# Optimization experiments

Hardware: AMD Instinct MI355X
Metric: run time of the kernel (lower is better)

Reference implementation:

```python
import jax, jax.numpy as jnp
import numpy as np

PC_RANGE = (-51.2, -51.2, -3.0, 51.2, 51.2, 1.0)
OUT = 3   # roi_align_size
SR = 2    # fixed sampling ratio (approximates mmcv adaptive sampling_ratio=0)


def roi_align_rotated(fm, rois_b, cx, cy, w, h, angle):
    """mmcv-style RoIAlignRotated, aligned=True, spatial_scale=1, clockwise=True.
    fm: [B,C,H,W]; rois_b int [N]; cx,cy,w,h,angle float [N]. Returns [N,C,OUT,OUT]."""
    B, C, H, W = fm.shape
    fm_hwc = jnp.transpose(fm, (0, 2, 3, 1))  # [B,H,W,C] for channel-last gather
    cx = cx - 0.5  # aligned=True pixel-center offset
    cy = cy - 0.5
    theta = -angle  # clockwise=True
    cos_t, sin_t = jnp.cos(theta), jnp.sin(theta)
    bin_h = h / OUT
    bin_w = w / OUT
    ph = jnp.arange(OUT, dtype=fm.dtype)
    sg = (jnp.arange(SR, dtype=fm.dtype) + 0.5) / SR
    # local (un-rotated) sample coords, [N, OUT, SR]
    yy = -h[:, None, None] / 2 + (ph[None, :, None] + sg[None, None, :]) * bin_h[:, None, None]
    xx = -w[:, None, None] / 2 + (ph[None, :, None] + sg[None, None, :]) * bin_w[:, None, None]
    # broadcast to [N, OUT(ph), OUT(pw), SR(iy), SR(ix)]
    yy = yy[:, :, None, :, None]
    xx = xx[:, None, :, None, :]
    c = cos_t[:, None, None, None, None]
    s = sin_t[:, None, None, None, None]
    y = yy * c - xx * s + cy[:, None, None, None, None]
    x = yy * s + xx * c + cx[:, None, None, None, None]
    N = cx.shape[0]
    P = OUT * OUT * SR * SR
    y = y.reshape(N, P)
    x = x.reshape(N, P)
    valid = (y > -1.0) & (y < H) & (x > -1.0) & (x < W)
    y = jnp.clip(y, 0.0, H - 1)
    x = jnp.clip(x, 0.0, W - 1)
    y0 = jnp.minimum(jnp.floor(y).astype(jnp.int32), H - 1)
    x0 = jnp.minimum(jnp.floor(x).astype(jnp.int32), W - 1)
    y1 = jnp.minimum(y0 + 1, H - 1)
    x1 = jnp.minimum(x0 + 1, W - 1)
    ly = y - y0
    lx = x - x0
    hy, hx = 1.0 - ly, 1.0 - lx
    bi = rois_b[:, None].astype(jnp.int32)
    v00 = fm_hwc[bi, y0, x0]  # [N,P,C]
    v01 = fm_hwc[bi, y0, x1]
    v10 = fm_hwc[bi, y1, x0]
    v11 = fm_hwc[bi, y1, x1]
    val = (hy * hx)[..., None] * v00 + (hy * lx)[..., None] * v01 \
        + (ly * hx)[..., None] * v10 + (ly * lx)[..., None] * v11
    val = val * valid[..., None].astype(fm.dtype)
    val = val.reshape(N, OUT, OUT, SR * SR, C).mean(axis=3)  # average over samples
    return jnp.transpose(val, (0, 3, 1, 2))  # [N,C,OUT,OUT]


def fc2(x, w1, w2):
    # two Conv1d(k=1, bias=False) + ReLU == two bias-free linears + ReLU
    return jax.nn.relu(jax.nn.relu(x @ w1.T) @ w2.T)


def setup_inputs() -> dict:
    key = jax.random.key(0)
    ks = jax.random.split(key, 20)
    B, C, H, W, N = 4, 256, 256, 256, 2048
    F = OUT * OUT * C  # 2304
    D = 256            # n_fc_neurons
    fm = jax.random.normal(ks[0], (B, C, H, W), jnp.float32)
    u = jax.random.uniform(ks[1], (N, 7), jnp.float32)
    boxes = jnp.stack([
        u[:, 0] * 90.0 - 45.0,        # x in [-45,45] m
        u[:, 1] * 90.0 - 45.0,        # y
        u[:, 2] * 2.0 - 2.0,          # z
        u[:, 3] * 4.5 + 1.5,          # h
        u[:, 4] * 4.5 + 1.5,          # w (roi height in pixels)
        u[:, 5] * 4.5 + 1.5,          # l (roi width in pixels)
        u[:, 6] * 2.0 * np.pi - np.pi  # yaw
    ], axis=1)
    bidx = jax.random.randint(ks[2], (N,), 0, B, dtype=jnp.int32)
    def mkw(k, o, i):
        return jax.random.normal(k, (o, i), jnp.float32) * np.float32(1.0 / np.sqrt(i))
    return {
        'feature_map': fm, 'boxes': boxes, 'batch_idx': bidx,
        'w_sh1': mkw(ks[3], D, F), 'w_sh2': mkw(ks[4], D, D),
        'w_cls1': mkw(ks[5], D, D), 'w_cls2': mkw(ks[6], D, D),
        'w_cls3': mkw(ks[7], 1, D), 'b_cls3': jnp.zeros((1,), jnp.float32),
        'w_iou1': mkw(ks[8], D, D), 'w_iou2': mkw(ks[9], D, D),
        'w_iou3': mkw(ks[10], 1, D), 'b_iou3': jnp.zeros((1,), jnp.float32),
        'w_reg1': mkw(ks[11], D, D), 'w_reg2': mkw(ks[12], D, D),
        'w_reg3': mkw(ks[13], 7, D) * np.float32(0.001), 'b_reg3': jnp.zeros((7,), jnp.float32),
    }


def reference(feature_map, boxes, batch_idx,
              w_sh1, w_sh2,
              w_cls1, w_cls2, w_cls3, b_cls3,
              w_iou1, w_iou2, w_iou3, b_iou3,
              w_reg1, w_reg2, w_reg3, b_reg3):
    H, W = feature_map.shape[2], feature_map.shape[3]
    gw = (PC_RANGE[3] - PC_RANGE[0]) / W
    gh = (PC_RANGE[4] - PC_RANGE[1]) / H
    cx = (boxes[:, 0] - PC_RANGE[0]) / gw
    cy = (boxes[:, 1] - PC_RANGE[1]) / gh
    rw = boxes[:, 5] / gw  # enlarge_ratio = 1
    rh = boxes[:, 4] / gh
    ang = boxes[:, 6]
    pooled = roi_align_rotated(feature_map, batch_idx, cx, cy, rw, rh, ang)  # [N,C,3,3]
    N, C = pooled.shape[0], pooled.shape[1]
    # flatten(2).permute(0,2,1).flatten(1): bin-major, channel-minor
    x = jnp.transpose(pooled.reshape(N, C, OUT * OUT), (0, 2, 1)).reshape(N, OUT * OUT * C)
    sh = fc2(x, w_sh1, w_sh2)
    rcnn_cls = fc2(sh, w_cls1, w_cls2) @ w_cls3.T + b_cls3
    rcnn_iou = fc2(sh, w_iou1, w_iou2) @ w_iou3.T + b_iou3
    rcnn_reg = fc2(sh, w_reg1, w_reg2) @ w_reg3.T + b_reg3
    return rcnn_cls, rcnn_iou, rcnn_reg
```

## Files before the change

### kernel.cpp

```cpp
#include <hip/hip_runtime.h>
#include <hip/hip_fp16.h>

typedef float f4v __attribute__((ext_vector_type(4)));
typedef _Float16 h4 __attribute__((ext_vector_type(4)));
typedef _Float16 h8 __attribute__((ext_vector_type(8)));

#define NROI 2048
#define NCH  256
#define MAPH 256
#define MAPW 256
#define HWSZ (MAPH*MAPW)
#define FDIM 2304
#define MN   (2048*256)

#define O_SH1 0
#define O_SH2 589824
#define O_C1  655360
#define O_C2  720896
#define O_I1  786432
#define O_I2  851968
#define O_R1  917504
#define O_R2  983040

__global__ __launch_bounds__(256) void convert_w_kernel(
    const float* __restrict__ s1, const float* __restrict__ s2,
    const float* __restrict__ c1, const float* __restrict__ c2,
    const float* __restrict__ i1, const float* __restrict__ i2,
    const float* __restrict__ r1, const float* __restrict__ r2,
    __half* __restrict__ wbuf)
{
    const int b = blockIdx.x, t = threadIdx.x;
    const float* src;
    int base;
    if (b < 1152) { src = s1 + (size_t)b*512; base = b*512; }
    else {
        int j  = (b - 1152) >> 7;
        int lb = (b - 1152) & 127;
        switch (j) {
            case 0: src = s2; break; case 1: src = c1; break;
            case 2: src = c2; break; case 3: src = i1; break;
            case 4: src = i2; break; case 5: src = r1; break;
            default: src = r2; break;
        }
        src += (size_t)lb*512;
        base = 589824 + (b - 1152)*512;
    }
    float2 v = *(const float2*)(src + t*2);
    *(__half2*)(wbuf + base + t*2) = __floats2half2_rn(v.x, v.y);
}

#define TP 136

__global__ __launch_bounds__(256) void transpose_kernel(
    const float* __restrict__ fm, __half* __restrict__ hwc)
{
    __shared__ _Float16 tile[128 * TP];
    const int tid = threadIdx.x;
    const int x0 = blockIdx.x * 128, c0 = blockIdx.y * 128;
    const int bz = blockIdx.z;
    const int b = bz >> 8, y = bz & 255;

    const int xh = tid & 31;
    const int cb = tid >> 5;
    const float* src = fm + (((size_t)b*NCH + c0 + cb)*MAPH + y)*MAPW + x0 + xh*4;
    const int swz = (xh & 15) << 2;
    const int xbase = xh * 4;

    #pragma unroll
    for (int p = 0; p < 16; p++) {
        f4v v = *(const f4v*)(src + (size_t)p*8*HWSZ);
        const int c = (cb + p*8) ^ swz;
        tile[(xbase+0)*TP + c] = (_Float16)v[0];
        tile[(xbase+1)*TP + c] = (_Float16)v[1];
        tile[(xbase+2)*TP + c] = (_Float16)v[2];
        tile[(xbase+3)*TP + c] = (_Float16)v[3];
    }
    __syncthreads();

    const int cq = tid & 31;
    const int xb = tid >> 5;
    __half* dst = hwc + (((size_t)b*MAPH + y)*MAPW + x0)*NCH + c0 + cq*4;
    #pragma unroll
    for (int it = 0; it < 16; it++) {
        int x = xb + it*8;
        h4 v = *(const h4*)&tile[x*TP + ((cq*4) ^ (((x>>2)&15) << 2))];
        *(h4*)(dst + (size_t)x*NCH) = v;
    }
}

__global__ __launch_bounds__(256) void roi_hwc_kernel(
    const __half* __restrict__ hwc, const float* __restrict__ boxes,
    const int* __restrict__ bidx, __half* __restrict__ xout)
{
    const int tid  = threadIdx.x;
    const int r    = tid >> 7;
    const int lt   = tid & 127;
    const int wq   = lt >> 6;
    const int lane = lt & 63;
    const int n    = blockIdx.x * 2 + r;

    __shared__ float sw[2][4][36];
    __shared__ int   soff[2][4][36];
    __shared__ int   sb[2];

    if (lt < 36) {
        float b0 = boxes[n*7+0], b1 = boxes[n*7+1];
        float b4 = boxes[n*7+4], b5 = boxes[n*7+5], b6 = boxes[n*7+6];
        float cx = (b0 + 51.2f) / 0.4f - 0.5f;
        float cy = (b1 + 51.2f) / 0.4f - 0.5f;
        float w  = b5 / 0.4f;
        float h  = b4 / 0.4f;
        float th = -b6;
        float ct = cosf(th), st = sinf(th);
        float binh = h / 3.0f, binw = w / 3.0f;
        int s  = lt;
        int ph = s / 12, pw = (s % 12) / 4, sy = (s % 4) / 2, sx = s & 1;
        float sgy = ((float)sy + 0.5f) * 0.5f;
        float sgx = ((float)sx + 0.5f) * 0.5f;
        float yy  = -h*0.5f + ((float)ph + sgy) * binh;
        float xxl = -w*0.5f + ((float)pw + sgx) * binw;
        float y = yy*ct - xxl*st + cy;
        float x = yy*st + xxl*ct + cx;
        bool valid = (y > -1.0f) && (y < 256.0f) && (x > -1.0f) && (x < 256.0f);
        y = fminf(fmaxf(y, 0.0f), 255.0f);
        x = fminf(fmaxf(x, 0.0f), 255.0f);
        int y0 = (int)floorf(y); if (y0 > 255) y0 = 255;
        int x0 = (int)floorf(x); if (x0 > 255) x0 = 255;
        int y1 = min(y0+1, 255), x1 = min(x0+1, 255);
        float ly = y - (float)y0, lx = x - (float)x0;
        float hy = 1.0f - ly, hx = 1.0f - lx;
        float v = valid ? 0.25f : 0.0f;
        sw[r][0][s] = hy*hx*v; sw[r][1][s] = hy*lx*v;
        sw[r][2][s] = ly*hx*v; sw[r][3][s] = ly*lx*v;
        soff[r][0][s] = (y0*MAPW + x0)*NCH;
        soff[r][1][s] = (y0*MAPW + x1)*NCH;
        soff[r][2][s] = (y1*MAPW + x0)*NCH;
        soff[r][3][s] = (y1*MAPW + x1)*NCH;
    }
    if (lt == 0) sb[r] = bidx[n];
    __syncthreads();

    const __half* base = hwc + (size_t)sb[r]*(HWSZ*NCH) + lane*4;
    __half* xo = xout + (size_t)n*FDIM + lane*4;

    for (int pp = wq; pp < 9; pp += 2) {
        float a0 = 0.f, a1 = 0.f, a2 = 0.f, a3 = 0.f;
        #pragma unroll
        for (int q = 0; q < 4; q++) {
            int s = pp*4 + q;
            #pragma unroll
            for (int cc = 0; cc < 4; cc++) {
                h4 v = *(const h4*)(base + soff[r][cc][s]);
                float wgt = sw[r][cc][s];
                a0 += wgt * (float)v[0];
                a1 += wgt * (float)v[1];
                a2 += wgt * (float)v[2];
                a3 += wgt * (float)v[3];
            }
        }
        h4 o; o[0]=(_Float16)a0; o[1]=(_Float16)a1; o[2]=(_Float16)a2; o[3]=(_Float16)a3;
        *(h4*)(xo + pp*NCH) = o;
    }
}

struct PtrsH {
    const __half* A[3];
    const __half* W[3];
    void* C[3];
};

__device__ inline h8 ldsH8(const _Float16* p) {
    h4 lo = *(const h4*)p;
    h4 hi = *(const h4*)(p + 4);
    return __builtin_shufflevector(lo, hi, 0,1,2,3,4,5,6,7);
}

template<bool RELU, bool SPLITK, bool OUTH>
__global__ __launch_bounds__(256) void gemm_h_kernel(PtrsH p, int M, int N, int K, int kChunk)
{
    __shared__ _Float16 As[64*40];
    __shared__ _Float16 Ws[64*40];
    const int z = blockIdx.z;
    const _Float16* A; const _Float16* W; void* C;
    int k0, k1;
    if (SPLITK) {
        A = (const _Float16*)p.A[0]; W = (const _Float16*)p.W[0];
        k0 = z * kChunk; k1 = k0 + kChunk;
        C = (char*)p.C[0] + (size_t)z * M * N * 4;
    } else {
        A = (const _Float16*)p.A[z]; W = (const _Float16*)p.W[z]; C = p.C[z];
        k0 = 0; k1 = K;
    }
    const int tid = threadIdx.x;
    const int m0 = blockIdx.x * 64, n0 = blockIdx.y * 64;
    const int srow = tid >> 2, skc = (tid & 3) * 8;
    const _Float16* Ald = A + (size_t)(m0 + srow) * K + k0 + skc;
    const _Float16* Wld = W + (size_t)(n0 + srow) * K + k0 + skc;
    const int wv = tid >> 6, lane = tid & 63;
    const int quad = lane >> 4, mr = lane & 15;

    f4v acc[4] = {};
    h8 aR = *(const h8*)Ald;
    h8 wR = *(const h8*)Wld;

    for (int kt = k0; kt < k1; kt += 32) {
        __syncthreads();
        *(h4*)&As[srow*40 + skc]     = __builtin_shufflevector(aR, aR, 0,1,2,3);
        *(h4*)&As[srow*40 + skc + 4] = __builtin_shufflevector(aR, aR, 4,5,6,7);
        *(h4*)&Ws[srow*40 + skc]     = __builtin_shufflevector(wR, wR, 0,1,2,3);
        *(h4*)&Ws[srow*40 + skc + 4] = __builtin_shufflevector(wR, wR, 4,5,6,7);
        __syncthreads();
        if (kt + 32 < k1) {
            Ald += 32; Wld += 32;
            aR = *(const h8*)Ald;
            wR = *(const h8*)Wld;
        }
        h8 af = ldsH8(&As[(wv*16 + mr)*40 + quad*8]);
        #pragma unroll
        for (int j = 0; j < 4; j++) {
            h8 bf = ldsH8(&Ws[(j*16 + mr)*40 + quad*8]);
            acc[j] = __builtin_amdgcn_mfma_f32_16x16x32_f16(af, bf, acc[j], 0, 0, 0);
        }
    }

    const int orow = m0 + wv*16 + quad*4;
    #pragma unroll
    for (int j = 0; j < 4; j++) {
        int col = n0 + j*16 + mr;
        #pragma unroll
        for (int rr = 0; rr < 4; rr++) {
            float v = acc[j][rr];
            if (RELU) v = fmaxf(v, 0.0f);
            if (OUTH) ((__half*)C)[(size_t)(orow + rr) * N + col] = __float2half(v);
            else      ((float*)C)[(size_t)(orow + rr) * N + col] = v;
        }
    }
}

__global__ __launch_bounds__(256) void reduce_relu_h_kernel(
    const float* __restrict__ pin, __half* __restrict__ hout)
{
    int i = blockIdx.x * 256 + threadIdx.x;
    const f4v* p4 = (const f4v*)pin;
    f4v a = p4[i];
    a += p4[i + MN/4];
    a += p4[i + 2*(MN/4)];
    a += p4[i + 3*(MN/4)];
    h4 o;
    #pragma unroll
    for (int j = 0; j < 4; j++) o[j] = (_Float16)fmaxf(a[j], 0.0f);
    *(h4*)(hout + (size_t)i*4) = o;
}

__global__ __launch_bounds__(256) void heads_kernel(
    const float* __restrict__ c2, const float* __restrict__ i2, const float* __restrict__ r2,
    const float* __restrict__ wc3, const float* __restrict__ bc3,
    const float* __restrict__ wi3, const float* __restrict__ bi3,
    const float* __restrict__ wr3, const float* __restrict__ br3,
    float* __restrict__ out)
{
    const int lane = threadIdx.x & 63;
    const int wv   = threadIdx.x >> 6;
    const int n    = blockIdx.x * 4 + wv;
    const float* cr = c2 + (size_t)n*256;
    const float* ir = i2 + (size_t)n*256;
    const float* rr = r2 + (size_t)n*256;
    float vc = 0.0f, vi = 0.0f, vr[7] = {};
    #pragma unroll
    for (int j = 0; j < 4; j++) {
        int k = lane + j*64;
        float cv = cr[k], iv = ir[k], rv = rr[k];
        vc += cv * wc3[k];
        vi += iv * wi3[k];
        #pragma unroll
        for (int t = 0; t < 7; t++) vr[t] += rv * wr3[t*256 + k];
    }
    #pragma unroll
    for (int off = 32; off > 0; off >>= 1) {
        vc += __shfl_down(vc, off, 64);
        vi += __shfl_down(vi, off, 64);
        #pragma unroll
        for (int t = 0; t < 7; t++) vr[t] += __shfl_down(vr[t], off, 64);
    }
    if (lane == 0) {
        out[n]        = vc + bc3[0];
        out[2048 + n] = vi + bi3[0];
        #pragma unroll
        for (int t = 0; t < 7; t++) out[4096 + n*7 + t] = vr[t] + br3[t];
    }
}

extern "C" void kernel_launch(void* const* d_in, const int* in_sizes, int n_in,
                              void* d_out, int out_size, void* d_ws, size_t ws_size,
                              hipStream_t stream)
{
    const float* fm    = (const float*)d_in[0];
    const float* boxes = (const float*)d_in[1];
    const int*   bidx  = (const int*)d_in[2];
    const float* w_sh1 = (const float*)d_in[3];
    const float* w_sh2 = (const float*)d_in[4];
    const float* w_c1  = (const float*)d_in[5];
    const float* w_c2  = (const float*)d_in[6];
    const float* w_c3  = (const float*)d_in[7];
    const float* b_c3  = (const float*)d_in[8];
    const float* w_i1  = (const float*)d_in[9];
    const float* w_i2  = (const float*)d_in[10];
    const float* w_i3  = (const float*)d_in[11];
    const float* b_i3  = (const float*)d_in[12];
    const float* w_r1  = (const float*)d_in[13];
    const float* w_r2  = (const float*)d_in[14];
    const float* w_r3  = (const float*)d_in[15];
    const float* b_r3  = (const float*)d_in[16];
    float* out = (float*)d_out;

    char* base = (char*)d_ws;
    __half* hwc  = (__half*)base;
    __half* xh   = (__half*)(base + (size_t)4*NCH*HWSZ*2);
    __half* h1h  = (__half*)((char*)xh + (size_t)NROI*FDIM*2);
    __half* shh  = (__half*)((char*)h1h + (size_t)MN*2);
    __half* b1c  = (__half*)((char*)shh + (size_t)MN*2);
    __half* b1i  = b1c + MN;
    __half* b1r  = b1i + MN;
    float*  b2c  = (float*)((char*)b1c + (size_t)3*MN*2);
    float*  b2i  = b2c + MN;
    float*  b2r  = b2i + MN;
    float*  part = (float*)((char*)b2c + (size_t)3*MN*4);
    __half* wbuf = (__half*)((char*)part + (size_t)4*MN*4);

    convert_w_kernel<<<2048, 256, 0, stream>>>(w_sh1, w_sh2, w_c1, w_c2,
                                               w_i1, w_i2, w_r1, w_r2, wbuf);
    transpose_kernel<<<dim3(2, 2, 4*MAPH), 256, 0, stream>>>(fm, hwc);
    roi_hwc_kernel<<<NROI/2, 256, 0, stream>>>(hwc, boxes, bidx, xh);

    PtrsH g1;
    g1.A[0]=g1.A[1]=g1.A[2]=xh;
    g1.W[0]=g1.W[1]=g1.W[2]=wbuf + O_SH1;
    g1.C[0]=g1.C[1]=g1.C[2]=part;
    gemm_h_kernel<false,true,false><<<dim3(32,4,4), 256, 0, stream>>>(g1, 2048, 256, 2304, 576);

    reduce_relu_h_kernel<<<MN/4/256, 256, 0, stream>>>(part, h1h);

    PtrsH g2;
    g2.A[0]=g2.A[1]=g2.A[2]=h1h;
    g2.W[0]=g2.W[1]=g2.W[2]=wbuf + O_SH2;
    g2.C[0]=g2.C[1]=g2.C[2]=shh;
    gemm_h_kernel<true,false,true><<<dim3(32,4,1), 256, 0, stream>>>(g2, 2048, 256, 256, 0);

    PtrsH g3;
    g3.A[0]=g3.A[1]=g3.A[2]=shh;
    g3.W[0]=wbuf + O_C1; g3.W[1]=wbuf + O_I1; g3.W[2]=wbuf + O_R1;
    g3.C[0]=b1c; g3.C[1]=b1i; g3.C[2]=b1r;
    gemm_h_kernel<true,false,true><<<dim3(32,4,3), 256, 0, stream>>>(g3, 2048, 256, 256, 0);

    PtrsH g4;
    g4.A[0]=b1c; g4.A[1]=b1i; g4.A[2]=b1r;
    g4.W[0]=wbuf + O_C2; g4.W[1]=wbuf + O_I2; g4.W[2]=wbuf + O_R2;
    g4.C[0]=b2c; g4.C[1]=b2i; g4.C[2]=b2r;
    gemm_h_kernel<true,false,false><<<dim3(32,4,3), 256, 0, stream>>>(g4, 2048, 256, 256, 0);

    heads_kernel<<<NROI/4, 256, 0, stream>>>(b2c, b2i, b2r,
                                             w_c3, b_c3, w_i3, b_i3, w_r3, b_r3, out);
}
```

Before: 472.1 us.

## Fuse final head projections into last GEMM epilogue with atomic accumulation

Removes the separate heads kernel and the fp32 intermediate buffers. The last hidden-layer GEMM now applies ReLU and immediately projects onto the final head weights in its epilogue. Partial sums are reduced across lanes and accumulated into the output with atomicAdd. Biases are written ahead of time by extra blocks in the weight-conversion kernel. This saves one launch and the write and read of the intermediate activations, at the cost of atomics, nondeterministic summation order and more register pressure in the reg-head epilogue.

```diff
diff --git a/kernel.cpp b/kernel.cpp
--- a/kernel.cpp
+++ b/kernel.cpp
@@ -27,9 +27,24 @@
     const float* __restrict__ c1, const float* __restrict__ c2,
     const float* __restrict__ i1, const float* __restrict__ i2,
     const float* __restrict__ r1, const float* __restrict__ r2,
-    __half* __restrict__ wbuf)
+    __half* __restrict__ wbuf,
+    const float* __restrict__ bc3, const float* __restrict__ bi3,
+    const float* __restrict__ br3, float* __restrict__ out)
 {
     const int b = blockIdx.x, t = threadIdx.x;
+    if (b >= 2048) {
+        int idx = (b - 2048) * 1024 + t * 4;
+        #pragma unroll
+        for (int k = 0; k < 4; k++) {
+            int i = idx + k;
+            float v;
+            if (i < 2048)      v = bc3[0];
+            else if (i < 4096) v = bi3[0];
+            else               v = br3[(i - 4096) % 7];
+            out[i] = v;
+        }
+        return;
+    }
     const float* src;
     int base;
     if (b < 1152) { src = s1 + (size_t)b*512; base = b*512; }
@@ -237,6 +252,103 @@
     }
 }
 
+__global__ __launch_bounds__(256) void gemm_heads_kernel(
+    const __half* __restrict__ Ac, const __half* __restrict__ Ai, const __half* __restrict__ Ar,
+    const __half* __restrict__ wbuf,
+    const float* __restrict__ wc3, const float* __restrict__ wi3, const float* __restrict__ wr3,
+    float* __restrict__ out)
+{
+    __shared__ _Float16 As[64*40];
+    __shared__ _Float16 Ws[64*40];
+    const int z = blockIdx.z;
+    const _Float16* A = (const _Float16*)(z == 0 ? Ac : (z == 1 ? Ai : Ar));
+    const _Float16* W = (const _Float16*)wbuf + (z == 0 ? O_C2 : (z == 1 ? O_I2 : O_R2));
+    const int K = 256;
+    const int tid = threadIdx.x;
+    const int m0 = blockIdx.x * 64, n0 = blockIdx.y * 64;
+    const int srow = tid >> 2, skc = (tid & 3) * 8;
+    const _Float16* Ald = A + (size_t)(m0 + srow) * K + skc;
+    const _Float16* Wld = W + (size_t)(n0 + srow) * K + skc;
+    const int wv = tid >> 6, lane = tid & 63;
+    const int quad = lane >> 4, mr = lane & 15;
+
+    f4v acc[4] = {};
+    h8 aR = *(const h8*)Ald;
+    h8 wR = *(const h8*)Wld;
+
+    for (int kt = 0; kt < K; kt += 32) {
+        __syncthreads();
+        *(h4*)&As[srow*40 + skc]     = __builtin_shufflevector(aR, aR, 0,1,2,3);
+        *(h4*)&As[srow*40 + skc + 4] = __builtin_shufflevector(aR, aR, 4,5,6,7);
+        *(h4*)&Ws[srow*40 + skc]     = __builtin_shufflevector(wR, wR, 0,1,2,3);
+        *(h4*)&Ws[srow*40 + skc + 4] = __builtin_shufflevector(wR, wR, 4,5,6,7);
+        __syncthreads();
+        if (kt + 32 < K) {
+            Ald += 32; Wld += 32;
+            aR = *(const h8*)Ald;
+            wR = *(const h8*)Wld;
+        }
+        h8 af = ldsH8(&As[(wv*16 + mr)*40 + quad*8]);
+        #pragma unroll
+        for (int j = 0; j < 4; j++) {
+            h8 bf = ldsH8(&Ws[(j*16 + mr)*40 + quad*8]);
+            acc[j] = __builtin_amdgcn_mfma_f32_16x16x32_f16(af, bf, acc[j], 0, 0, 0);
+        }
+    }
+
+    const int orow = m0 + wv*16 + quad*4;
+    if (z < 2) {
+        const float* w3 = (z == 0) ? wc3 : wi3;
+        float pc[4] = {0.f, 0.f, 0.f, 0.f};
+        #pragma unroll
+        for (int j = 0; j < 4; j++) {
+            float w3v = w3[n0 + j*16 + mr];
+            #pragma unroll
+            for (int rr = 0; rr < 4; rr++)
+                pc[rr] += fmaxf(acc[j][rr], 0.0f) * w3v;
+        }
+        #pragma unroll
+        for (int off = 1; off < 16; off <<= 1) {
+            #pragma unroll
+            for (int rr = 0; rr < 4; rr++)
+                pc[rr] += __shfl_xor(pc[rr], off, 64);
+        }
+        if (mr == 0) {
+            #pragma unroll
+            for (int rr = 0; rr < 4; rr++)
+                atomicAdd(out + z*2048 + orow + rr, pc[rr]);
+        }
+    } else {
+        float pr[4][7] = {};
+        #pragma unroll
+        for (int j = 0; j < 4; j++) {
+            int col = n0 + j*16 + mr;
+            #pragma unroll
+            for (int rr = 0; rr < 4; rr++) {
+                float v = fmaxf(acc[j][rr], 0.0f);
+                #pragma unroll
+                for (int t = 0; t < 7; t++)
+                    pr[rr][t] += v * wr3[t*256 + col];
+            }
+        }
+        #pragma unroll
+        for (int off = 1; off < 16; off <<= 1) {
+            #pragma unroll
+            for (int rr = 0; rr < 4; rr++)
+                #pragma unroll
+                for (int t = 0; t < 7; t++)
+                    pr[rr][t] += __shfl_xor(pr[rr][t], off, 64);
+        }
+        if (mr == 0) {
+            #pragma unroll
+            for (int rr = 0; rr < 4; rr++)
+                #pragma unroll
+                for (int t = 0; t < 7; t++)
+                    atomicAdd(out + 4096 + (size_t)(orow + rr)*7 + t, pr[rr][t]);
+        }
+    }
+}
+
 __global__ __launch_bounds__(256) void reduce_relu_h_kernel(
     const float* __restrict__ pin, __half* __restrict__ hout)
 {
@@ -250,44 +362,6 @@
     #pragma unroll
     for (int j = 0; j < 4; j++) o[j] = (_Float16)fmaxf(a[j], 0.0f);
     *(h4*)(hout + (size_t)i*4) = o;
-}
-
-__global__ __launch_bounds__(256) void heads_kernel(
-    const float* __restrict__ c2, const float* __restrict__ i2, const float* __restrict__ r2,
-    const float* __restrict__ wc3, const float* __restrict__ bc3,
-    const float* __restrict__ wi3, const float* __restrict__ bi3,
-    const float* __restrict__ wr3, const float* __restrict__ br3,
-    float* __restrict__ out)
-{
-    const int lane = threadIdx.x & 63;
-    const int wv   = threadIdx.x >> 6;
-    const int n    = blockIdx.x * 4 + wv;
-    const float* cr = c2 + (size_t)n*256;
-    const float* ir = i2 + (size_t)n*256;
-    const float* rr = r2 + (size_t)n*256;
-    float vc = 0.0f, vi = 0.0f, vr[7] = {};
-    #pragma unroll
-    for (int j = 0; j < 4; j++) {
-        int k = lane + j*64;
-        float cv = cr[k], iv = ir[k], rv = rr[k];
-        vc += cv * wc3[k];
-        vi += iv * wi3[k];
-        #pragma unroll
-        for (int t = 0; t < 7; t++) vr[t] += rv * wr3[t*256 + k];
-    }
-    #pragma unroll
-    for (int off = 32; off > 0; off >>= 1) {
-        vc += __shfl_down(vc, off, 64);
-        vi += __shfl_down(vi, off, 64);
-        #pragma unroll
-        for (int t = 0; t < 7; t++) vr[t] += __shfl_down(vr[t], off, 64);
-    }
-    if (lane == 0) {
-        out[n]        = vc + bc3[0];
-        out[2048 + n] = vi + bi3[0];
-        #pragma unroll
-        for (int t = 0; t < 7; t++) out[4096 + n*7 + t] = vr[t] + br3[t];
-    }
 }
 
 extern "C" void kernel_launch(void* const* d_in, const int* in_sizes, int n_in,
@@ -321,14 +395,12 @@
     __half* b1c  = (__half*)((char*)shh + (size_t)MN*2);
     __half* b1i  = b1c + MN;
     __half* b1r  = b1i + MN;
-    float*  b2c  = (float*)((char*)b1c + (size_t)3*MN*2);
-    float*  b2i  = b2c + MN;
-    float*  b2r  = b2i + MN;
-    float*  part = (float*)((char*)b2c + (size_t)3*MN*4);
+    float*  part = (float*)((char*)b1c + (size_t)3*MN*2);
     __half* wbuf = (__half*)((char*)part + (size_t)4*MN*4);
 
-    convert_w_kernel<<<2048, 256, 0, stream>>>(w_sh1, w_sh2, w_c1, w_c2,
-                                               w_i1, w_i2, w_r1, w_r2, wbuf);
+    convert_w_kernel<<<2066, 256, 0, stream>>>(w_sh1, w_sh2, w_c1, w_c2,
+                                               w_i1, w_i2, w_r1, w_r2, wbuf,
+                                               b_c3, b_i3, b_r3, out);
     transpose_kernel<<<dim3(2, 2, 4*MAPH), 256, 0, stream>>>(fm, hwc);
     roi_hwc_kernel<<<NROI/2, 256, 0, stream>>>(hwc, boxes, bidx, xh);
 
@@ -352,12 +424,6 @@
     g3.C[0]=b1c; g3.C[1]=b1i; g3.C[2]=b1r;
     gemm_h_kernel<true,false,true><<<dim3(32,4,3), 256, 0, stream>>>(g3, 2048, 256, 256, 0);
 
-    PtrsH g4;
-    g4.A[0]=b1c; g4.A[1]=b1i; g4.A[2]=b1r;
-    g4.W[0]=wbuf + O_C2; g4.W[1]=wbuf + O_I2; g4.W[2]=wbuf + O_R2;
-    g4.C[0]=b2c; g4.C[1]=b2i; g4.C[2]=b2r;
-    gemm_h_kernel<true,false,false><<<dim3(32,4,3), 256, 0, stream>>>(g4, 2048, 256, 256, 0);
-
-    heads_kernel<<<NROI/4, 256, 0, stream>>>(b2c, b2i, b2r,
-                                             w_c3, b_c3, w_i3, b_i3, w_r3, b_r3, out);
-}
+    gemm_heads_kernel<<<dim3(32,4,3), 256, 0, stream>>>(b1c, b1i, b1r, wbuf,
+                                                        w_c3, w_i3, w_r3, out);
+}
```

Result: no change. 472.8 us (+0.1%).
